# Optimization experiments

Measured on AMD Instinct MI355X. Metric: run time of the kernel, lower is better.

## Reference

```python
import jax, jax.numpy as jnp
import numpy as np

TEMPERATURE = 0.5
EPS = 1e-8  # torch F.cosine_similarity eps


def setup_inputs() -> dict:
    key = jax.random.key(0)
    k1, k2 = jax.random.split(key)
    aug_hidden1 = jax.random.normal(k1, (4096, 512), dtype=jnp.float32)
    aug_hidden2 = jax.random.normal(k2, (4096, 512), dtype=jnp.float32)
    return {"aug_hidden1": aug_hidden1, "aug_hidden2": aug_hidden2}


def reference(aug_hidden1, aug_hidden2):
    B = aug_hidden1.shape[0]
    z = jnp.concatenate([aug_hidden1, aug_hidden2], axis=0)  # [2B, D]
    # cosine similarity == normalize rows (with eps clamp) then GEMM
    norms = jnp.sqrt(jnp.sum(z * z, axis=1, keepdims=True))
    z = z / jnp.maximum(norms, EPS)
    sim = z @ z.T  # [2B, 2B]
    n = 2 * B
    diag_mask = jnp.eye(n, dtype=bool)
    sim = jnp.where(diag_mask, -jnp.inf, sim)
    # positives: diag offsets +B and -B
    pos = jnp.concatenate([jnp.diagonal(sim, offset=B), jnp.diagonal(sim, offset=-B)], axis=0)  # [2B]
    # -log(exp(pos/T) / sum_j exp(sim/T)) = -pos/T + logsumexp(sim/T)
    lse = jax.nn.logsumexp(sim / TEMPERATURE, axis=1)  # diag -inf contributes exp=0
    loss = -(pos / TEMPERATURE) + lse
    return loss.mean()
```

## Files before the change

kernel.cpp:

```cpp
#include <hip/hip_runtime.h>
#include <hip/hip_bf16.h>

typedef float f32x4 __attribute__((ext_vector_type(4)));
typedef long  lx2   __attribute__((ext_vector_type(2)));

#define B_ROWS 4096
#define NROWS  8192
#define DDIM   512
#define SCALE2 2.8853900817779268f


__global__ __launch_bounds__(256) void normalize_kernel(
    const float* __restrict__ h1, const float* __restrict__ h2,
    unsigned char* __restrict__ zq, float* __restrict__ out) {
  __shared__ __align__(16) unsigned char tile[8192];
  if (blockIdx.x == 0 && threadIdx.x == 0) out[0] = 0.0f;

  const int wave = threadIdx.x >> 6;
  const int lane = threadIdx.x & 63;
  const int rg = blockIdx.x;
  const int G = lane >> 3, g8 = lane & 7;
  const int quad = g8 & 3, half = g8 >> 2;

  #pragma unroll
  for (int it = 0; it < 4; ++it) {
    const int r = it * 4 + wave;
    const int row = rg * 16 + r;
    const float* src = (row < B_ROWS) ? (h1 + (size_t)row * DDIM)
                                      : (h2 + (size_t)(row - B_ROWS) * DDIM);
    float4 v0 = *(const float4*)(src + lane * 8);
    float4 v1 = *(const float4*)(src + lane * 8 + 4);
    float ss = v0.x*v0.x + v0.y*v0.y + v0.z*v0.z + v0.w*v0.w
             + v1.x*v1.x + v1.y*v1.y + v1.z*v1.z + v1.w*v1.w;
    #pragma unroll
    for (int m = 1; m <= 32; m <<= 1) ss += __shfl_xor(ss, m);
    float sc = 1.0f / fmaxf(sqrtf(ss), 1e-8f);
    int lo = 0, hi = 0;
    lo = __builtin_amdgcn_cvt_pk_fp8_f32(v0.x*sc, v0.y*sc, lo, 0);
    lo = __builtin_amdgcn_cvt_pk_fp8_f32(v0.z*sc, v0.w*sc, lo, 1);
    hi = __builtin_amdgcn_cvt_pk_fp8_f32(v1.x*sc, v1.y*sc, hi, 0);
    hi = __builtin_amdgcn_cvt_pk_fp8_f32(v1.z*sc, v1.w*sc, hi, 1);
    *(int2*)(tile + G * 1024 + (quad * 16 + r) * 16 + half * 8) = make_int2(lo, hi);
  }
  __syncthreads();
  int4 w0 = *(const int4*)(tile + threadIdx.x * 16);
  int4 w1 = *(const int4*)(tile + 4096 + threadIdx.x * 16);
  *(int4*)(zq + (size_t)rg * 8192 + threadIdx.x * 16) = w0;
  *(int4*)(zq + (size_t)rg * 8192 + 4096 + threadIdx.x * 16) = w1;
}

__global__ __launch_bounds__(256, 4) void simexp_kernel(
    const unsigned char* __restrict__ zq, float* __restrict__ scratch,
    float* __restrict__ pos) {
  __shared__ __align__(16) unsigned char As[16384];
  __shared__ __align__(16) unsigned char Bs[16384];
  __shared__ float rp[256];
  __shared__ float cp[256];

  const int tid  = threadIdx.x;
  const int wave = tid >> 6;
  const int lane = tid & 63;
  const int wm = wave >> 1, wn = wave & 1;
  const int quad = lane >> 4;
  const int l16  = lane & 15;

  int t  = blockIdx.x;
  int bi = (int)((sqrtf(8.0f * (float)t + 1.0f) - 1.0f) * 0.5f);
  while ((bi + 1) * (bi + 2) / 2 <= t) ++bi;
  while (bi * (bi + 1) / 2 > t) --bi;
  int bj = t - bi * (bi + 1) / 2;
  const int rowBlk = bi * 128;
  const int colBlk = bj * 128;
  const bool isDiag = (bi == bj);

  const unsigned char* aBase = zq + (size_t)bi * 65536;
  const unsigned char* bBase = zq + (size_t)bj * 65536;

  f32x4 acc[4][4] = {};

  #pragma unroll
  for (int h = 0; h < 4; ++h) {
    if (h) __syncthreads();
    #pragma unroll
    for (int i = 0; i < 4; ++i) {
      const int s = wave * 4 + i;
      const int rg = s >> 1, gl = s & 1;
      const size_t goff = (size_t)(rg * 8 + h * 2 + gl) * 1024 + lane * 16;
      __builtin_amdgcn_global_load_lds(
          (const __attribute__((address_space(1))) unsigned int*)(aBase + goff),
          (__attribute__((address_space(3))) unsigned int*)(As + s * 1024), 16, 0, 0);
      __builtin_amdgcn_global_load_lds(
          (const __attribute__((address_space(1))) unsigned int*)(bBase + goff),
          (__attribute__((address_space(3))) unsigned int*)(Bs + s * 1024), 16, 0, 0);
    }
    __syncthreads();

    #pragma unroll
    for (int gl = 0; gl < 2; ++gl) {
      lx2 afr[4], bfr[4];
      #pragma unroll
      for (int rt = 0; rt < 4; ++rt)
        afr[rt] = *(const lx2*)(As + (size_t)((wm * 4 + rt) * 2 + gl) * 1024 + lane * 16);
      #pragma unroll
      for (int ct = 0; ct < 4; ++ct)
        bfr[ct] = *(const lx2*)(Bs + (size_t)((wn * 4 + ct) * 2 + gl) * 1024 + lane * 16);
      #pragma unroll
      for (int rt = 0; rt < 4; ++rt)
        #pragma unroll
        for (int ct = 0; ct < 4; ++ct) {
          acc[rt][ct] = __builtin_amdgcn_mfma_f32_16x16x32_fp8_fp8(
              afr[rt].x, bfr[ct].x, acc[rt][ct], 0, 0, 0);
          acc[rt][ct] = __builtin_amdgcn_mfma_f32_16x16x32_fp8_fp8(
              afr[rt].y, bfr[ct].y, acc[rt][ct], 0, 0, 0);
        }
    }
  }

  const bool posBlk = (bi - bj == 32);
  float colpart[4] = {0.f, 0.f, 0.f, 0.f};
  #pragma unroll
  for (int rt = 0; rt < 4; ++rt) {
    #pragma unroll
    for (int r = 0; r < 4; ++r) {
      const int lrow = wm * 64 + rt * 16 + quad * 4 + r;
      const int grow = rowBlk + lrow;
      float s = 0.f;
      #pragma unroll
      for (int ct = 0; ct < 4; ++ct) {
        const int gcol = colBlk + wn * 64 + ct * 16 + l16;
        float sv = acc[rt][ct][r];
        float e = exp2f(sv * SCALE2);
        if (isDiag && grow == gcol) e = 0.f;
        if (posBlk && grow - B_ROWS == gcol) pos[gcol] = sv;
        s += e;
        colpart[ct] += e;
      }
      s += __shfl_xor(s, 1);
      s += __shfl_xor(s, 2);
      s += __shfl_xor(s, 4);
      s += __shfl_xor(s, 8);
      if (l16 == 0) rp[lrow * 2 + wn] = s;
    }
  }
  #pragma unroll
  for (int ct = 0; ct < 4; ++ct) {
    float c = colpart[ct];
    c += __shfl_xor(c, 16);
    c += __shfl_xor(c, 32);
    if (quad == 0) cp[(wn * 64 + ct * 16 + l16) * 2 + wm] = c;
  }
  __syncthreads();
  if (tid < 128) {
    scratch[(size_t)(bi * 64 + bj) * 128 + tid] = rp[tid * 2] + rp[tid * 2 + 1];
  } else if (!isDiag) {
    const int c = tid - 128;
    scratch[(size_t)(bj * 64 + bi) * 128 + c] = cp[c * 2] + cp[c * 2 + 1];
  }
}

__global__ __launch_bounds__(256) void finalize_kernel(
    const float* __restrict__ scratch, const float* __restrict__ pos,
    float* __restrict__ out) {
  __shared__ float red[4];
  const int gid = blockIdx.x * 256 + threadIdx.x;
  const int band = gid >> 7, r = gid & 127;
  const float* base = scratch + (size_t)band * 64 * 128 + r;
  float s = 0.f;
  #pragma unroll 8
  for (int c = 0; c < 64; ++c) s += base[c * 128];
  float loss = __logf(s) - 2.0f * pos[gid & (B_ROWS - 1)];
  #pragma unroll
  for (int m = 1; m <= 32; m <<= 1) loss += __shfl_xor(loss, m);
  const int wave = threadIdx.x >> 6;
  const int lane = threadIdx.x & 63;
  if (lane == 0) red[wave] = loss;
  __syncthreads();
  if (threadIdx.x == 0)
    atomicAdd(out, (red[0] + red[1] + red[2] + red[3]) * (1.0f / NROWS));
}

extern "C" void kernel_launch(void* const* d_in, const int* in_sizes, int n_in,
                              void* d_out, int out_size, void* d_ws, size_t ws_size,
                              hipStream_t stream) {
  const float* h1 = (const float*)d_in[0];
  const float* h2 = (const float*)d_in[1];
  float* out = (float*)d_out;
  unsigned char* zq = (unsigned char*)d_ws;
  float* scratch = (float*)((char*)d_ws + (size_t)NROWS * DDIM);
  float* pos     = scratch + 64 * 64 * 128;

  normalize_kernel<<<NROWS / 16, 256, 0, stream>>>(h1, h2, zq, out);
  simexp_kernel<<<64 * 65 / 2, 256, 0, stream>>>(zq, scratch, pos);
  finalize_kernel<<<NROWS / 256, 256, 0, stream>>>(scratch, pos, out);
}
```

Before: 50.20 us.

## Switch FP8 GEMM to 32x32x64 scaled MFMA with matching operand layout

Replaces the 16x16x32 fp8 MFMA pairs with the gfx950 scaled 32x32x64 f8f6f4 MFMA using unit scales. The normalize kernel writes a new 32-row tiled fp8 layout, the LDS staging and fragment loads change to 32-byte per-lane reads, and the epilogue is remapped to the 32x32 accumulator layout. The aim is fewer MFMA issues and LDS reads per FLOP, with higher matrix throughput per instruction. In exchange the remapping of row and column indices in the epilogue is more complex and must match the instruction's register layout exactly.

After: 134.7 us. 2.68x slower.

```diff
diff --git a/kernel.cpp b/kernel.cpp
--- a/kernel.cpp
+++ b/kernel.cpp
@@ -1,31 +1,32 @@
 #include <hip/hip_runtime.h>
-#include <hip/hip_bf16.h>
 
-typedef float f32x4 __attribute__((ext_vector_type(4)));
-typedef long  lx2   __attribute__((ext_vector_type(2)));
+typedef int   i32x8  __attribute__((ext_vector_type(8)));
+typedef float f32x16 __attribute__((ext_vector_type(16)));
 
 #define B_ROWS 4096
 #define NROWS  8192
 #define DDIM   512
 #define SCALE2 2.8853900817779268f
+#define SCL1   0x7f7f7f7f
 
 
 __global__ __launch_bounds__(256) void normalize_kernel(
     const float* __restrict__ h1, const float* __restrict__ h2,
     unsigned char* __restrict__ zq, float* __restrict__ out) {
-  __shared__ __align__(16) unsigned char tile[8192];
+  __shared__ __align__(16) unsigned char tile[16384];
   if (blockIdx.x == 0 && threadIdx.x == 0) out[0] = 0.0f;
 
   const int wave = threadIdx.x >> 6;
   const int lane = threadIdx.x & 63;
-  const int rg = blockIdx.x;
-  const int G = lane >> 3, g8 = lane & 7;
-  const int quad = g8 & 3, half = g8 >> 2;
+  const int rb = blockIdx.x;
+  const int kg   = lane >> 3;
+  const int h    = (lane >> 2) & 1;
+  const int koff = (lane & 3) * 8;
 
   #pragma unroll
-  for (int it = 0; it < 4; ++it) {
+  for (int it = 0; it < 8; ++it) {
     const int r = it * 4 + wave;
-    const int row = rg * 16 + r;
+    const int row = rb * 32 + r;
     const float* src = (row < B_ROWS) ? (h1 + (size_t)row * DDIM)
                                       : (h2 + (size_t)(row - B_ROWS) * DDIM);
     float4 v0 = *(const float4*)(src + lane * 8);
@@ -40,13 +41,14 @@
     lo = __builtin_amdgcn_cvt_pk_fp8_f32(v0.z*sc, v0.w*sc, lo, 1);
     hi = __builtin_amdgcn_cvt_pk_fp8_f32(v1.x*sc, v1.y*sc, hi, 0);
     hi = __builtin_amdgcn_cvt_pk_fp8_f32(v1.z*sc, v1.w*sc, hi, 1);
-    *(int2*)(tile + G * 1024 + (quad * 16 + r) * 16 + half * 8) = make_int2(lo, hi);
+    *(int2*)(tile + kg * 2048 + h * 1024 + r * 32 + koff) = make_int2(lo, hi);
   }
   __syncthreads();
-  int4 w0 = *(const int4*)(tile + threadIdx.x * 16);
-  int4 w1 = *(const int4*)(tile + 4096 + threadIdx.x * 16);
-  *(int4*)(zq + (size_t)rg * 8192 + threadIdx.x * 16) = w0;
-  *(int4*)(zq + (size_t)rg * 8192 + 4096 + threadIdx.x * 16) = w1;
+  const size_t base = (size_t)rb * 16384;
+  #pragma unroll
+  for (int j = 0; j < 4; ++j)
+    *(int4*)(zq + base + j * 4096 + threadIdx.x * 16) =
+        *(const int4*)(tile + j * 4096 + threadIdx.x * 16);
 }
 
 __global__ __launch_bounds__(256, 4) void simexp_kernel(
@@ -61,8 +63,8 @@
   const int wave = tid >> 6;
   const int lane = tid & 63;
   const int wm = wave >> 1, wn = wave & 1;
-  const int quad = lane >> 4;
-  const int l16  = lane & 15;
+  const int l31 = lane & 31;
+  const int hi5 = lane >> 5;
 
   int t  = blockIdx.x;
   int bi = (int)((sqrtf(8.0f * (float)t + 1.0f) - 1.0f) * 0.5f);
@@ -76,59 +78,59 @@
   const unsigned char* aBase = zq + (size_t)bi * 65536;
   const unsigned char* bBase = zq + (size_t)bj * 65536;
 
-  f32x4 acc[4][4] = {};
+  f32x16 acc[2][2] = {};
 
   #pragma unroll
   for (int h = 0; h < 4; ++h) {
     if (h) __syncthreads();
     #pragma unroll
     for (int i = 0; i < 4; ++i) {
-      const int s = wave * 4 + i;
-      const int rg = s >> 1, gl = s & 1;
-      const size_t goff = (size_t)(rg * 8 + h * 2 + gl) * 1024 + lane * 16;
+      const int u = wave * 4 + i;
+      const int s = u >> 1;
+      const int rg32 = s >> 1, gl = s & 1;
+      const size_t goff =
+          (size_t)((rg32 * 8 + h * 2 + gl) * 2048 + (u & 1) * 1024 + lane * 16);
+      const size_t loff = (size_t)(u * 1024 + lane * 16);
       __builtin_amdgcn_global_load_lds(
           (const __attribute__((address_space(1))) unsigned int*)(aBase + goff),
-          (__attribute__((address_space(3))) unsigned int*)(As + s * 1024), 16, 0, 0);
+          (__attribute__((address_space(3))) unsigned int*)(As + loff), 16, 0, 0);
       __builtin_amdgcn_global_load_lds(
           (const __attribute__((address_space(1))) unsigned int*)(bBase + goff),
-          (__attribute__((address_space(3))) unsigned int*)(Bs + s * 1024), 16, 0, 0);
+          (__attribute__((address_space(3))) unsigned int*)(Bs + loff), 16, 0, 0);
     }
     __syncthreads();
 
     #pragma unroll
     for (int gl = 0; gl < 2; ++gl) {
-      lx2 afr[4], bfr[4];
+      i32x8 afr[2], bfr[2];
       #pragma unroll
-      for (int rt = 0; rt < 4; ++rt)
-        afr[rt] = *(const lx2*)(As + (size_t)((wm * 4 + rt) * 2 + gl) * 1024 + lane * 16);
+      for (int rt = 0; rt < 2; ++rt)
+        afr[rt] = *(const i32x8*)(As + (size_t)((wm * 2 + rt) * 2 + gl) * 2048 + lane * 32);
       #pragma unroll
-      for (int ct = 0; ct < 4; ++ct)
-        bfr[ct] = *(const lx2*)(Bs + (size_t)((wn * 4 + ct) * 2 + gl) * 1024 + lane * 16);
+      for (int ct = 0; ct < 2; ++ct)
+        bfr[ct] = *(const i32x8*)(Bs + (size_t)((wn * 2 + ct) * 2 + gl) * 2048 + lane * 32);
       #pragma unroll
-      for (int rt = 0; rt < 4; ++rt)
+      for (int rt = 0; rt < 2; ++rt)
         #pragma unroll
-        for (int ct = 0; ct < 4; ++ct) {
-          acc[rt][ct] = __builtin_amdgcn_mfma_f32_16x16x32_fp8_fp8(
-              afr[rt].x, bfr[ct].x, acc[rt][ct], 0, 0, 0);
-          acc[rt][ct] = __builtin_amdgcn_mfma_f32_16x16x32_fp8_fp8(
-              afr[rt].y, bfr[ct].y, acc[rt][ct], 0, 0, 0);
-        }
+        for (int ct = 0; ct < 2; ++ct)
+          acc[rt][ct] = __builtin_amdgcn_mfma_scale_f32_32x32x64_f8f6f4(
+              afr[rt], bfr[ct], acc[rt][ct], 0, 0, 0, SCL1, 0, SCL1);
     }
   }
 
   const bool posBlk = (bi - bj == 32);
-  float colpart[4] = {0.f, 0.f, 0.f, 0.f};
+  float colpart[2] = {0.f, 0.f};
   #pragma unroll
-  for (int rt = 0; rt < 4; ++rt) {
+  for (int rt = 0; rt < 2; ++rt) {
     #pragma unroll
-    for (int r = 0; r < 4; ++r) {
-      const int lrow = wm * 64 + rt * 16 + quad * 4 + r;
+    for (int reg = 0; reg < 16; ++reg) {
+      const int lrow = wm * 64 + rt * 32 + (reg & 3) + 8 * (reg >> 2) + 4 * hi5;
       const int grow = rowBlk + lrow;
       float s = 0.f;
       #pragma unroll
-      for (int ct = 0; ct < 4; ++ct) {
-        const int gcol = colBlk + wn * 64 + ct * 16 + l16;
-        float sv = acc[rt][ct][r];
+      for (int ct = 0; ct < 2; ++ct) {
+        const int gcol = colBlk + wn * 64 + ct * 32 + l31;
+        float sv = acc[rt][ct][reg];
         float e = exp2f(sv * SCALE2);
         if (isDiag && grow == gcol) e = 0.f;
         if (posBlk && grow - B_ROWS == gcol) pos[gcol] = sv;
@@ -139,15 +141,15 @@
       s += __shfl_xor(s, 2);
       s += __shfl_xor(s, 4);
       s += __shfl_xor(s, 8);
-      if (l16 == 0) rp[lrow * 2 + wn] = s;
+      s += __shfl_xor(s, 16);
+      if (l31 == 0) rp[lrow * 2 + wn] = s;
     }
   }
   #pragma unroll
-  for (int ct = 0; ct < 4; ++ct) {
+  for (int ct = 0; ct < 2; ++ct) {
     float c = colpart[ct];
-    c += __shfl_xor(c, 16);
     c += __shfl_xor(c, 32);
-    if (quad == 0) cp[(wn * 64 + ct * 16 + l16) * 2 + wm] = c;
+    if (hi5 == 0) cp[(wn * 64 + ct * 32 + l31) * 2 + wm] = c;
   }
   __syncthreads();
   if (tid < 128) {
@@ -189,7 +191,7 @@
   float* scratch = (float*)((char*)d_ws + (size_t)NROWS * DDIM);
   float* pos     = scratch + 64 * 64 * 128;
 
-  normalize_kernel<<<NROWS / 16, 256, 0, stream>>>(h1, h2, zq, out);
+  normalize_kernel<<<NROWS / 32, 256, 0, stream>>>(h1, h2, zq, out);
   simexp_kernel<<<64 * 65 / 2, 256, 0, stream>>>(zq, scratch, pos);
   finalize_kernel<<<NROWS / 256, 256, 0, stream>>>(scratch, pos, out);
 }
```
